# Optimization experiments

Hardware: AMD Instinct MI355X
Metric: run time of the kernel (lower is better)

## Reference

```python
import jax, jax.numpy as jnp
import numpy as np

N_HEAD = 16
D_HEAD = 64
D_MODEL = 1024
QLEN = 1024
BSZ = 4
RLEN = 1024
CONV = 7
SCALE = 1.0 / D_HEAD ** 0.5
NEG = -1e30
EPS = 1e-5


def setup_inputs() -> dict:
    key = jax.random.key(0)
    ks = jax.random.split(key, 14)
    s = 0.02
    inp = {
        "w": jax.random.normal(ks[0], (QLEN, BSZ, D_MODEL), jnp.float32),
        "r": jax.random.normal(ks[1], (RLEN, D_MODEL), jnp.float32),
        "r_w_bias": jax.random.normal(ks[2], (N_HEAD, D_HEAD), jnp.float32) * s,
        "r_r_bias": jax.random.normal(ks[3], (N_HEAD, D_HEAD), jnp.float32) * s,
        "W_qkv": jax.random.normal(ks[4], (3 * N_HEAD * D_HEAD, D_MODEL), jnp.float32) * s,
        "W_r": jax.random.normal(ks[5], (N_HEAD * D_HEAD, D_MODEL), jnp.float32) * s,
        "W_o": jax.random.normal(ks[6], (D_MODEL, N_HEAD * D_HEAD), jnp.float32) * s,
        "conv_wq": jax.random.normal(ks[7], (D_HEAD, D_HEAD, CONV), jnp.float32) * s,
        "conv_bq": jax.random.normal(ks[8], (D_HEAD,), jnp.float32) * s,
        "conv_wk": jax.random.normal(ks[9], (D_HEAD, D_HEAD, CONV), jnp.float32) * s,
        "conv_bk": jax.random.normal(ks[10], (D_HEAD,), jnp.float32) * s,
        "conv_wv": jax.random.normal(ks[11], (D_HEAD, D_HEAD, CONV), jnp.float32) * s,
        "conv_bv": jax.random.normal(ks[12], (D_HEAD,), jnp.float32) * s,
        "ln_gamma": jnp.ones((D_MODEL,), jnp.float32),
        "ln_beta": jnp.zeros((D_MODEL,), jnp.float32),
        # causal mask, True = masked out (original dim==3 branch: [qlen, klen, 1])
        "attn_mask": jnp.triu(jnp.ones((QLEN, QLEN), bool), k=1)[:, :, None],
    }
    return inp


def _conv1d(x, wgt, b):
    # x: [N, C, L], wgt: [O, I, K] (torch Conv1d layout), same padding
    y = jax.lax.conv_general_dilated(x, wgt, (1,), [(CONV // 2, CONV // 2)],
                                     dimension_numbers=("NCH", "OIH", "NCH"))
    return y + b[None, :, None]


def _rel_shift(x):
    # x: [q, k, b, n] -> Transformer-XL relative shift
    q, k, b, n = x.shape
    xp = jnp.concatenate([jnp.zeros((q, 1, b, n), x.dtype), x], axis=1)
    return xp.reshape(k + 1, q, b, n)[1:].reshape(q, k, b, n)


def reference(w, r, r_w_bias, r_r_bias, W_qkv, W_r, W_o,
              conv_wq, conv_bq, conv_wk, conv_bk, conv_wv, conv_bv,
              ln_gamma, ln_beta, attn_mask):
    qlen, bsz, _ = w.shape
    klen = qlen  # mems=None

    heads = jnp.einsum('qbm,hm->qbh', w, W_qkv)  # [q, b, 3*n*d]
    hq, hk, hv = jnp.split(heads, 3, axis=-1)

    def to_conv(x, L):
        # [L, b, n*d] -> [n*b, d, L]
        return x.reshape(L, bsz, N_HEAD, D_HEAD).transpose(2, 1, 3, 0).reshape(N_HEAD * bsz, D_HEAD, L)

    def from_conv(x, L):
        # [n*b, d, L] -> [L, b, n, d]
        return x.reshape(N_HEAD, bsz, D_HEAD, L).transpose(3, 1, 0, 2)

    q_h = from_conv(_conv1d(to_conv(hq, qlen), conv_wq, conv_bq), qlen)
    k_h = from_conv(_conv1d(to_conv(hk, klen), conv_wk, conv_bk), klen)
    v_h = from_conv(_conv1d(to_conv(hv, klen), conv_wv, conv_bv), klen)

    r_head_k = (r @ W_r.T).reshape(-1, N_HEAD, D_HEAD)  # [rlen, n, d]

    AC = jnp.einsum('ibnd,jbnd->ijbn', q_h + r_w_bias, k_h)
    BD = _rel_shift(jnp.einsum('ibnd,jnd->ijbn', q_h + r_r_bias, r_head_k))
    score = (AC + BD) * SCALE
    score = jnp.where(attn_mask[:, :, :, None], NEG, score)

    prob = jax.nn.softmax(score, axis=1)
    vec = jnp.einsum('ijbn,jbnd->ibnd', prob, v_h).reshape(qlen, bsz, N_HEAD * D_HEAD)
    attn_out = vec @ W_o.T

    x = w + attn_out
    mu = jnp.mean(x, axis=-1, keepdims=True)
    var = jnp.mean(jnp.square(x - mu), axis=-1, keepdims=True)
    return (x - mu) / jnp.sqrt(var + EPS) * ln_gamma + ln_beta
```

## Files before the change

kernel.cpp:

```cpp
#include <hip/hip_runtime.h>
#include <math.h>

#define L 1024
#define SCALEF 0.125f
#define NEGF -1e30f

typedef unsigned short u16;
typedef __bf16 bf16x8 __attribute__((ext_vector_type(8)));
typedef float f32x4 __attribute__((ext_vector_type(4)));
typedef unsigned short u16x8 __attribute__((ext_vector_type(8)));
typedef unsigned short u16x4 __attribute__((ext_vector_type(4)));

#define MFMA(a, b, c) __builtin_amdgcn_mfma_f32_16x16x32_bf16(a, b, c, 0, 0, 0)

__device__ inline u16 f2b(float f) {
  union { float f; unsigned u; } v; v.f = f;
  unsigned r = v.u + 0x7fffu + ((v.u >> 16) & 1u);
  return (u16)(r >> 16);
}

__device__ __forceinline__ void ld16(u16* lds, const u16* g) {
  __builtin_amdgcn_global_load_lds((const __attribute__((address_space(1))) unsigned int*)g,
                                   (__attribute__((address_space(3))) unsigned int*)lds, 16, 0, 0);
}

__global__ __launch_bounds__(256) void prep(const float* __restrict__ w, const float* __restrict__ Wqkv,
                                            const float* __restrict__ r, const float* __restrict__ Wr,
                                            const float* __restrict__ Wo,
                                            const float* __restrict__ cwq, const float* __restrict__ cwk,
                                            const float* __restrict__ cwv,
                                            u16* w_bf, u16* wqkv_bf, u16* r_bf, u16* wr_bf, u16* wo_bf,
                                            u16* wTq, u16* wTk, u16* wTv) {
  int i = blockIdx.x * 256 + threadIdx.x;
  if (i < 2621440) {
    const float* s; u16* d; int off;
    if (i < 1048576)      { s = w;    d = w_bf;    off = i; }
    else if (i < 1835008) { s = Wqkv; d = wqkv_bf; off = i - 1048576; }
    else if (i < 2097152) { s = r;    d = r_bf;    off = i - 1835008; }
    else if (i < 2359296) { s = Wr;   d = wr_bf;   off = i - 2097152; }
    else                  { s = Wo;   d = wo_bf;   off = i - 2359296; }
    float4 v = ((const float4*)s)[off];
    u16x4 o = {f2b(v.x), f2b(v.y), f2b(v.z), f2b(v.w)};
    ((u16x4*)d)[off] = o;
  } else {
    int j = i - 2621440;
    if (j < 86016) {
      int z = j / 28672, rem = j % 28672;
      const float* src = z == 0 ? cwq : z == 1 ? cwk : cwv;
      u16* dst = z == 0 ? wTq : z == 1 ? wTk : wTv;
      int tt = rem >> 12, rem2 = rem & 4095;
      int dout = rem2 >> 6, din = rem2 & 63;
      dst[rem] = f2b(src[(dout * 64 + din) * 7 + tt]);
    }
  }
}

template <int OB>
__device__ __forceinline__ void gemm_tile(u16* sA, u16* sB, const u16* A, const u16* B,
                                          void* Cp, int N, int K, int m0, int n0) {
  int t = threadIdx.x;
  int w = t >> 6, lane = t & 63;
  int q4 = lane >> 4, li = lane & 15;
  int mw = (w & 1) << 6, nw = (w >> 1) << 6;
  f32x4 acc[4][4];
#pragma unroll
  for (int i = 0; i < 4; ++i)
#pragma unroll
    for (int j = 0; j < 4; ++j) acc[i][j] = (f32x4){0.f, 0.f, 0.f, 0.f};
  int r0 = t >> 2, c0 = (t & 3) << 3;
  const u16* Ap0 = A + (size_t)(m0 + r0) * K + c0;
  const u16* Ap1 = A + (size_t)(m0 + 64 + r0) * K + c0;
  const u16* Bp0 = B + (size_t)(n0 + r0) * K + c0;
  const u16* Bp1 = B + (size_t)(n0 + 64 + r0) * K + c0;
  int wo512 = w * 512;
  ld16(sA + wo512, Ap0);
  ld16(sA + wo512 + 2048, Ap1);
  ld16(sB + wo512, Bp0);
  ld16(sB + wo512 + 2048, Bp1);
  int cur = 0;
  for (int kb = 0; kb < K; kb += 32) {
    __syncthreads();
    int nxt = cur ^ 1;
    if (kb + 32 < K) {
      u16* nA = sA + nxt * 4096;
      u16* nB = sB + nxt * 4096;
      ld16(nA + wo512, Ap0 + kb + 32);
      ld16(nA + wo512 + 2048, Ap1 + kb + 32);
      ld16(nB + wo512, Bp0 + kb + 32);
      ld16(nB + wo512 + 2048, Bp1 + kb + 32);
    }
    const u16* cA = sA + cur * 4096;
    const u16* cB = sB + cur * 4096;
    bf16x8 fa[4], fb[4];
#pragma unroll
    for (int i = 0; i < 4; ++i) fa[i] = *(const bf16x8*)&cA[(mw + i * 16 + li) * 32 + q4 * 8];
#pragma unroll
    for (int i = 0; i < 4; ++i) fb[i] = *(const bf16x8*)&cB[(nw + i * 16 + li) * 32 + q4 * 8];
#pragma unroll
    for (int mt = 0; mt < 4; ++mt)
#pragma unroll
      for (int nt = 0; nt < 4; ++nt) acc[mt][nt] = MFMA(fa[mt], fb[nt], acc[mt][nt]);
    cur = nxt;
  }
#pragma unroll
  for (int mt = 0; mt < 4; ++mt)
#pragma unroll
    for (int r = 0; r < 4; ++r) {
      size_t row = m0 + mw + mt * 16 + q4 * 4 + r;
      if (OB) {
        u16* C = (u16*)Cp;
#pragma unroll
        for (int nt = 0; nt < 4; ++nt) C[row * N + n0 + nw + nt * 16 + li] = f2b(acc[mt][nt][r]);
      } else {
        float* C = (float*)Cp;
#pragma unroll
        for (int nt = 0; nt < 4; ++nt) C[row * N + n0 + nw + nt * 16 + li] = acc[mt][nt][r];
      }
    }
}

__global__ __launch_bounds__(256) void gemm_stage1(const u16* __restrict__ w_bf, const u16* __restrict__ wqkv_bf,
                                                   u16* __restrict__ heads,
                                                   const u16* __restrict__ r_bf, const u16* __restrict__ wr_bf,
                                                   u16* __restrict__ rhk) {
  __shared__ u16 sA[2 * 128 * 32];
  __shared__ u16 sB[2 * 128 * 32];
  int id = blockIdx.x;
  if (id < 768) {
    gemm_tile<1>(sA, sB, w_bf, wqkv_bf, heads, 3072, 1024, (id / 24) << 7, (id % 24) << 7);
  } else {
    int j = id - 768;
    gemm_tile<1>(sA, sB, r_bf, wr_bf, rhk, 1024, 1024, (j >> 3) << 7, (j & 7) << 7);
  }
}

__global__ __launch_bounds__(256) void gemm_wo(const u16* __restrict__ A, const u16* __restrict__ B,
                                               float* __restrict__ C) {
  __shared__ u16 sA[2 * 64 * 32];
  __shared__ u16 sB[2 * 128 * 32];
  int t = threadIdx.x;
  int w = t >> 6, lane = t & 63;
  int q4 = lane >> 4, li = lane & 15;
  int m0 = blockIdx.y << 6, n0 = blockIdx.x << 7;
  int nw = w << 5;
  const int N = 1024, K = 1024;
  f32x4 acc[4][2];
#pragma unroll
  for (int i = 0; i < 4; ++i)
#pragma unroll
    for (int j = 0; j < 2; ++j) acc[i][j] = (f32x4){0.f, 0.f, 0.f, 0.f};
  int r0 = t >> 2, c0 = (t & 3) << 3;
  const u16* Ap = A + (size_t)(m0 + r0) * K + c0;
  const u16* Bp0 = B + (size_t)(n0 + r0) * K + c0;
  const u16* Bp1 = B + (size_t)(n0 + 64 + r0) * K + c0;
  int wo512 = w * 512;
  ld16(sA + wo512, Ap);
  ld16(sB + wo512, Bp0);
  ld16(sB + wo512 + 2048, Bp1);
  int cur = 0;
  for (int kb = 0; kb < K; kb += 32) {
    __syncthreads();
    int nxt = cur ^ 1;
    if (kb + 32 < K) {
      u16* nA = sA + nxt * 2048;
      u16* nB = sB + nxt * 4096;
      ld16(nA + wo512, Ap + kb + 32);
      ld16(nB + wo512, Bp0 + kb + 32);
      ld16(nB + wo512 + 2048, Bp1 + kb + 32);
    }
    const u16* cA = sA + cur * 2048;
    const u16* cB = sB + cur * 4096;
    bf16x8 fa[4], fb[2];
#pragma unroll
    for (int i = 0; i < 4; ++i) fa[i] = *(const bf16x8*)&cA[(i * 16 + li) * 32 + q4 * 8];
#pragma unroll
    for (int j = 0; j < 2; ++j) fb[j] = *(const bf16x8*)&cB[(nw + j * 16 + li) * 32 + q4 * 8];
#pragma unroll
    for (int mt = 0; mt < 4; ++mt)
#pragma unroll
      for (int nt = 0; nt < 2; ++nt) acc[mt][nt] = MFMA(fa[mt], fb[nt], acc[mt][nt]);
    cur = nxt;
  }
#pragma unroll
  for (int mt = 0; mt < 4; ++mt)
#pragma unroll
    for (int r = 0; r < 4; ++r) {
      size_t row = m0 + mt * 16 + q4 * 4 + r;
#pragma unroll
      for (int nt = 0; nt < 2; ++nt) C[row * N + n0 + nw + nt * 16 + li] = acc[mt][nt][r];
    }
}

__global__ __launch_bounds__(256) void conv3(const u16* __restrict__ x,
                                             const u16* __restrict__ wTq, const u16* __restrict__ wTk,
                                             const u16* __restrict__ wTv,
                                             const float* __restrict__ cbq, const float* __restrict__ cbk,
                                             const float* __restrict__ cbv,
                                             u16* __restrict__ qh, u16* __restrict__ kh, u16* __restrict__ vtg) {
  __shared__ u16 sX[70 * 72];
  int z = blockIdx.z;
  const u16* wT = z == 0 ? wTq : z == 1 ? wTk : wTv;
  const float* bias = z == 0 ? cbq : z == 1 ? cbk : cbv;
  int t = threadIdx.x;
  int w = t >> 6, lane = t & 63;
  int q4 = lane >> 4, li = lane & 15;
  int l0 = blockIdx.x << 6, bn = blockIdx.y;
  int b = bn >> 4, n = bn & 15;
  const u16* xb = x + b * 3072 + z * 1024 + n * 64;
  for (int e = t; e < 560; e += 256) {
    int ro = e >> 3, c = e & 7;
    int l = l0 - 3 + ro;
    u16x8 v = {0, 0, 0, 0, 0, 0, 0, 0};
    if (l >= 0 && l < L) v = *(const u16x8*)(xb + (size_t)l * 12288 + c * 8);
    *(u16x8*)&sX[ro * 72 + c * 8] = v;
  }
  bf16x8 Bw[7][2];
#pragma unroll
  for (int tt = 0; tt < 7; ++tt)
#pragma unroll
    for (int kc = 0; kc < 2; ++kc)
      Bw[tt][kc] = *(const bf16x8*)(wT + (tt * 64 + w * 16 + li) * 64 + kc * 32 + q4 * 8);
  f32x4 acc[4];
#pragma unroll
  for (int i = 0; i < 4; ++i) acc[i] = (f32x4){0.f, 0.f, 0.f, 0.f};
  __syncthreads();
#pragma unroll
  for (int tt = 0; tt < 7; ++tt)
#pragma unroll
    for (int kc = 0; kc < 2; ++kc)
#pragma unroll
      for (int mt = 0; mt < 4; ++mt) {
        bf16x8 a = *(const bf16x8*)&sX[(mt * 16 + li + tt) * 72 + kc * 32 + q4 * 8];
        acc[mt] = MFMA(a, Bw[tt][kc], acc[mt]);
      }
  float bv = bias[w * 16 + li];
  if (z < 2) {
    u16* out = z == 0 ? qh : kh;
#pragma unroll
    for (int mt = 0; mt < 4; ++mt)
#pragma unroll
      for (int r = 0; r < 4; ++r) {
        int l = l0 + mt * 16 + q4 * 4 + r;
        out[(((size_t)l * 4 + b) * 16 + n) * 64 + w * 16 + li] = f2b(acc[mt][r] + bv);
      }
  } else {
    __syncthreads();
#pragma unroll
    for (int mt = 0; mt < 4; ++mt)
#pragma unroll
      for (int r = 0; r < 4; ++r)
        sX[(w * 16 + li) * 72 + mt * 16 + q4 * 4 + r] = f2b(acc[mt][r] + bv);
    __syncthreads();
    int d = t >> 2, ch = t & 3;
    u16x8 v0 = *(u16x8*)&sX[d * 72 + ch * 16];
    u16x8 v1 = *(u16x8*)&sX[d * 72 + ch * 16 + 8];
    u16* dst = vtg + ((size_t)bn * 64 + d) * 1024 + l0 + ch * 16;
    *(u16x8*)dst = v0;
    *(u16x8*)(dst + 8) = v1;
  }
}

__global__ __launch_bounds__(256) void rel_attn(const u16* __restrict__ qh, const u16* __restrict__ kh,
                                                const u16* __restrict__ vt, const u16* __restrict__ rhk,
                                                const float* __restrict__ rwb_, const float* __restrict__ rrb_,
                                                u16* __restrict__ vec) {
  __shared__ u16 sK[64][72];
  __shared__ u16 sVt[64][72];
  __shared__ u16 sR[128][72];
  __shared__ u16 sP[4][16][72];
  int t = threadIdx.x;
  int w = t >> 6, lane = t & 63;
  int q4 = lane >> 4, li = lane & 15;
  int p = blockIdx.x, bn = blockIdx.y;
  int b = bn >> 4, n = bn & 15;
  int base_w = 48 - w * 16;
  const u16* vtb = vt + (size_t)bn * 64 * 1024;
  int er0 = t >> 3, ec = (t & 7) * 8;
  bf16x8 vone;
#pragma unroll
  for (int j = 0; j < 8; ++j) vone[j] = (__bf16)1.0f;
  float rwbv[2][8], rrbv[2][8];
#pragma unroll
  for (int kc = 0; kc < 2; ++kc)
#pragma unroll
    for (int j = 0; j < 8; ++j) {
      int d = kc * 32 + q4 * 8 + j;
      rwbv[kc][j] = rwb_[n * 64 + d];
      rrbv[kc][j] = rrb_[n * 64 + d];
    }
  for (int half = 0; half < 2; ++half) {
    int qt = (half == 0) ? p : 15 - p;
    int i0 = qt << 6;
    bf16x8 Aw[2], Ar[2];
    {
      const u16* qrow = qh + (((size_t)(i0 + w * 16 + li) * 4 + b) * 16 + n) * 64;
#pragma unroll
      for (int kc = 0; kc < 2; ++kc) {
        bf16x8 qv = *(const bf16x8*)(qrow + kc * 32 + q4 * 8);
        bf16x8 aw, ar;
#pragma unroll
        for (int j = 0; j < 8; ++j) {
          float qf = (float)qv[j];
          aw[j] = (__bf16)(qf + rwbv[kc][j]);
          ar[j] = (__bf16)(qf + rrbv[kc][j]);
        }
        Aw[kc] = aw;
        Ar[kc] = ar;
      }
    }
    f32x4 accO[4];
#pragma unroll
    for (int i = 0; i < 4; ++i) accO[i] = (f32x4){0.f, 0.f, 0.f, 0.f};
    f32x4 accL = (f32x4){0.f, 0.f, 0.f, 0.f};
    int ntile = qt + 1;
    u16x8 pK[2], pV[2], pR[4];
    {
      int j0 = 0, gB = 960 - i0;
#pragma unroll
      for (int i = 0; i < 2; ++i) {
        int row = er0 + i * 32;
        pK[i] = *(const u16x8*)(kh + (((size_t)(j0 + row) * 4 + b) * 16 + n) * 64 + ec);
        pV[i] = *(const u16x8*)(vtb + (size_t)row * 1024 + j0 + ec);
      }
#pragma unroll
      for (int i = 0; i < 4; ++i) {
        int m = er0 + i * 32;
        int g = gB + m;
        if (g > L - 1) g = L - 1;
        pR[i] = *(const u16x8*)(rhk + (size_t)g * 1024 + n * 64 + ec);
      }
    }
    for (int jt = 0; jt < ntile; ++jt) {
      __syncthreads();
#pragma unroll
      for (int i = 0; i < 2; ++i) {
        *(u16x8*)&sK[er0 + i * 32][ec] = pK[i];
        *(u16x8*)&sVt[er0 + i * 32][ec] = pV[i];
      }
#pragma unroll
      for (int i = 0; i < 4; ++i) *(u16x8*)&sR[er0 + i * 32][ec] = pR[i];
      __syncthreads();
      if (jt + 1 < ntile) {
        int j0 = (jt + 1) << 6, gB = 960 - i0 + j0;
#pragma unroll
        for (int i = 0; i < 2; ++i) {
          int row = er0 + i * 32;
          pK[i] = *(const u16x8*)(kh + (((size_t)(j0 + row) * 4 + b) * 16 + n) * 64 + ec);
          pV[i] = *(const u16x8*)(vtb + (size_t)row * 1024 + j0 + ec);
        }
#pragma unroll
        for (int i = 0; i < 4; ++i) {
          int m = er0 + i * 32;
          int g = gB + m;
          if (g > L - 1) g = L - 1;
          pR[i] = *(const u16x8*)(rhk + (size_t)g * 1024 + n * 64 + ec);
        }
      }
      int j0 = jt << 6;
      f32x4 accS[4], accG[5];
#pragma unroll
      for (int i = 0; i < 4; ++i) accS[i] = (f32x4){0.f, 0.f, 0.f, 0.f};
#pragma unroll
      for (int i = 0; i < 5; ++i) accG[i] = (f32x4){0.f, 0.f, 0.f, 0.f};
      __builtin_amdgcn_s_setprio(1);
#pragma unroll
      for (int kc = 0; kc < 2; ++kc) {
#pragma unroll
        for (int nt = 0; nt < 4; ++nt) {
          bf16x8 fk = *(const bf16x8*)&sK[nt * 16 + li][kc * 32 + q4 * 8];
          accS[nt] = MFMA(Aw[kc], fk, accS[nt]);
        }
#pragma unroll
        for (int nt = 0; nt < 5; ++nt) {
          bf16x8 fr = *(const bf16x8*)&sR[base_w + nt * 16 + li][kc * 32 + q4 * 8];
          accG[nt] = MFMA(Ar[kc], fr, accG[nt]);
        }
      }
      __builtin_amdgcn_s_setprio(0);
      float Sv[4][4];
#pragma unroll
      for (int nt = 0; nt < 4; ++nt)
#pragma unroll
        for (int r = 0; r < 4; ++r) {
          int il = q4 * 4 + r;
          int srcc = li + 15 - il;
          int lsrc = (lane & 48) | (srcc & 15);
          float pm = (li >= 15 - il) ? accG[nt][r] : accG[nt + 1][r];
          float g = __shfl(pm, lsrc);
          Sv[nt][r] = (accS[nt][r] + g) * SCALEF;
        }
      if (jt == qt) {
#pragma unroll
        for (int nt = 0; nt < 4; ++nt)
#pragma unroll
          for (int r = 0; r < 4; ++r)
            if (j0 + nt * 16 + li > i0 + w * 16 + q4 * 4 + r) Sv[nt][r] = NEGF;
      }
#pragma unroll
      for (int nt = 0; nt < 4; ++nt)
#pragma unroll
        for (int r = 0; r < 4; ++r) {
          float pv = __expf(Sv[nt][r]);
          sP[w][q4 * 4 + r][(nt * 16 + li) ^ (q4 << 3)] = f2b(pv);
        }
      __builtin_amdgcn_s_setprio(1);
#pragma unroll
      for (int kc = 0; kc < 2; ++kc) {
        bf16x8 ap = *(const bf16x8*)&sP[w][li][kc * 32 + ((q4 ^ ((li >> 2) & 3)) << 3)];
        accL = MFMA(ap, vone, accL);
#pragma unroll
        for (int nt = 0; nt < 4; ++nt) {
          bf16x8 fv = *(const bf16x8*)&sVt[nt * 16 + li][kc * 32 + q4 * 8];
          accO[nt] = MFMA(ap, fv, accO[nt]);
        }
      }
      __builtin_amdgcn_s_setprio(0);
    }
#pragma unroll
    for (int r = 0; r < 4; ++r) {
      int il = q4 * 4 + r;
      int ig = i0 + w * 16 + il;
      float inv = 1.0f / accL[r];
      u16* orow = vec + (((size_t)ig * 4 + b) * 16 + n) * 64;
#pragma unroll
      for (int nt = 0; nt < 4; ++nt) orow[nt * 16 + li] = f2b(accO[nt][r] * inv);
    }
  }
}

__global__ __launch_bounds__(256) void resid_ln(const float* __restrict__ w,
                                                const float* __restrict__ attn,
                                                const float* __restrict__ gamma,
                                                const float* __restrict__ beta,
                                                float* __restrict__ out) {
  __shared__ float ssum[4], ssq[4];
  int row = blockIdx.x, t = threadIdx.x;
  float4 xw = *(const float4*)&w[(size_t)row * 1024 + t * 4];
  float4 xa = *(const float4*)&attn[(size_t)row * 1024 + t * 4];
  float4 x = make_float4(xw.x + xa.x, xw.y + xa.y, xw.z + xa.z, xw.w + xa.w);
  float s = x.x + x.y + x.z + x.w;
  float sq = x.x * x.x + x.y * x.y + x.z * x.z + x.w * x.w;
#pragma unroll
  for (int off = 32; off > 0; off >>= 1) {
    s += __shfl_down(s, off);
    sq += __shfl_down(sq, off);
  }
  int wid = t >> 6;
  if ((t & 63) == 0) { ssum[wid] = s; ssq[wid] = sq; }
  __syncthreads();
  s = ssum[0] + ssum[1] + ssum[2] + ssum[3];
  sq = ssq[0] + ssq[1] + ssq[2] + ssq[3];
  float mean = s * (1.0f / 1024.0f);
  float var = sq * (1.0f / 1024.0f) - mean * mean;
  float rstd = rsqrtf(var + 1e-5f);
  float4 g = *(const float4*)&gamma[t * 4];
  float4 bb = *(const float4*)&beta[t * 4];
  float4 o;
  o.x = (x.x - mean) * rstd * g.x + bb.x;
  o.y = (x.y - mean) * rstd * g.y + bb.y;
  o.z = (x.z - mean) * rstd * g.z + bb.z;
  o.w = (x.w - mean) * rstd * g.w + bb.w;
  *(float4*)&out[(size_t)row * 1024 + t * 4] = o;
}

extern "C" void kernel_launch(void* const* d_in, const int* in_sizes, int n_in,
                              void* d_out, int out_size, void* d_ws, size_t ws_size,
                              hipStream_t stream) {
  const float* w     = (const float*)d_in[0];
  const float* r     = (const float*)d_in[1];
  const float* rwb   = (const float*)d_in[2];
  const float* rrb   = (const float*)d_in[3];
  const float* W_qkv = (const float*)d_in[4];
  const float* W_r   = (const float*)d_in[5];
  const float* W_o   = (const float*)d_in[6];
  const float* cwq   = (const float*)d_in[7];
  const float* cbq   = (const float*)d_in[8];
  const float* cwk   = (const float*)d_in[9];
  const float* cbk   = (const float*)d_in[10];
  const float* cwv   = (const float*)d_in[11];
  const float* cbv   = (const float*)d_in[12];
  const float* gamma = (const float*)d_in[13];
  const float* beta  = (const float*)d_in[14];
  float* outp = (float*)d_out;

  char* wsb = (char*)d_ws;
  u16*   heads   = (u16*)(wsb);
  u16*   vec     = (u16*)(wsb);
  float* attnf   = (float*)(wsb + 8388608);
  u16*   qh      = (u16*)(wsb + 25165824);
  u16*   kh      = (u16*)(wsb + 33554432);
  u16*   rhk     = (u16*)(wsb + 50331648);
  u16*   w_bf    = (u16*)(wsb + 52428800);
  u16*   wqkv_bf = (u16*)(wsb + 60817408);
  u16*   r_bf    = (u16*)(wsb + 67108864);
  u16*   wr_bf   = (u16*)(wsb + 69206016);
  u16*   wo_bf   = (u16*)(wsb + 71303168);
  u16*   wTq     = (u16*)(wsb + 73400320);
  u16*   wTk     = (u16*)(wsb + 73457664);
  u16*   wTv     = (u16*)(wsb + 73515008);
  u16*   vt      = (u16*)(wsb + 73572352);

  dim3 blk(256);
  prep<<<10576, blk, 0, stream>>>(w, W_qkv, r, W_r, W_o, cwq, cwk, cwv,
                                  w_bf, wqkv_bf, r_bf, wr_bf, wo_bf, wTq, wTk, wTv);
  gemm_stage1<<<832, blk, 0, stream>>>(w_bf, wqkv_bf, heads, r_bf, wr_bf, rhk);
  conv3<<<dim3(16, 64, 3), blk, 0, stream>>>(heads, wTq, wTk, wTv, cbq, cbk, cbv, qh, kh, vt);
  rel_attn<<<dim3(8, 64), blk, 0, stream>>>(qh, kh, vt, rhk, rwb, rrb, vec);
  gemm_wo<<<dim3(8, 64), blk, 0, stream>>>(vec, wo_bf, attnf);
  resid_ln<<<4096, blk, 0, stream>>>(w, attnf, gamma, beta, outp);
}
```

Measured before the change: 261.9 us.

## Rewrite stage-1 GEMM with 256x256 tiles, 4-stage LDS pipeline and swizzle

Replaces the 128x128 double-buffered GEMM tile for the QKV and R projections with a 256x256 tile computed by 512 threads (8 waves). It uses a 4-slot LDS ring with explicit vmcnt waits, an XOR swizzle on LDS columns to avoid bank conflicts, and s_setprio around the MFMA bursts. The aim is more data reuse per loaded byte and better overlap of global loads with MFMA. In exchange the grid drops to 208 blocks, fewer than two per CU, and the kernel uses 128KB of LDS per block with one block per CU, so load balance and occupancy may suffer.

```diff
diff --git a/kernel.cpp b/kernel.cpp
--- a/kernel.cpp
+++ b/kernel.cpp
@@ -56,81 +56,97 @@
 }
 
 template <int OB>
-__device__ __forceinline__ void gemm_tile(u16* sA, u16* sB, const u16* A, const u16* B,
-                                          void* Cp, int N, int K, int m0, int n0) {
+__device__ __forceinline__ void gemm256_tile(u16* lds, const u16* __restrict__ A,
+                                             const u16* __restrict__ B, void* Cp,
+                                             int N, int m0, int n0) {
   int t = threadIdx.x;
-  int w = t >> 6, lane = t & 63;
+  int wv = t >> 6, lane = t & 63;
   int q4 = lane >> 4, li = lane & 15;
-  int mw = (w & 1) << 6, nw = (w >> 1) << 6;
-  f32x4 acc[4][4];
-#pragma unroll
-  for (int i = 0; i < 4; ++i)
-#pragma unroll
-    for (int j = 0; j < 4; ++j) acc[i][j] = (f32x4){0.f, 0.f, 0.f, 0.f};
-  int r0 = t >> 2, c0 = (t & 3) << 3;
-  const u16* Ap0 = A + (size_t)(m0 + r0) * K + c0;
-  const u16* Ap1 = A + (size_t)(m0 + 64 + r0) * K + c0;
-  const u16* Bp0 = B + (size_t)(n0 + r0) * K + c0;
-  const u16* Bp1 = B + (size_t)(n0 + 64 + r0) * K + c0;
-  int wo512 = w * 512;
-  ld16(sA + wo512, Ap0);
-  ld16(sA + wo512 + 2048, Ap1);
-  ld16(sB + wo512, Bp0);
-  ld16(sB + wo512 + 2048, Bp1);
-  int cur = 0;
-  for (int kb = 0; kb < K; kb += 32) {
-    __syncthreads();
-    int nxt = cur ^ 1;
-    if (kb + 32 < K) {
-      u16* nA = sA + nxt * 4096;
-      u16* nB = sB + nxt * 4096;
-      ld16(nA + wo512, Ap0 + kb + 32);
-      ld16(nA + wo512 + 2048, Ap1 + kb + 32);
-      ld16(nB + wo512, Bp0 + kb + 32);
-      ld16(nB + wo512 + 2048, Bp1 + kb + 32);
-    }
-    const u16* cA = sA + cur * 4096;
-    const u16* cB = sB + cur * 4096;
+  int wm = wv >> 2, wn = wv & 3;
+  int pc = (q4 ^ ((li >> 1) & 3)) << 3;
+  int cs = (((t & 3) ^ ((t >> 3) & 3)) << 3);
+  const u16* Ab = A + (size_t)(m0 + (t >> 2)) * 1024 + cs;
+  const u16* Bb = B + (size_t)(n0 + (t >> 2)) * 1024 + cs;
+  int wo = wv * 512;
+  f32x4 acc[8][4];
+#pragma unroll
+  for (int m = 0; m < 8; ++m)
+#pragma unroll
+    for (int n = 0; n < 4; ++n) acc[m][n] = (f32x4){0.f, 0.f, 0.f, 0.f};
+#define STAGE_A(kt) { int sl = ((kt) & 3) * 16384, kb = (kt) * 32; \
+    ld16(lds + sl + wo, Ab + kb); ld16(lds + sl + 4096 + wo, Ab + 131072 + kb); }
+#define STAGE_B(kt) { int sl = ((kt) & 3) * 16384 + 8192, kb = (kt) * 32; \
+    ld16(lds + sl + wo, Bb + kb); ld16(lds + sl + 4096 + wo, Bb + 131072 + kb); }
+  STAGE_A(0); STAGE_B(0); STAGE_A(1); STAGE_B(1);
+  asm volatile("s_waitcnt vmcnt(4)" ::: "memory");
+  __builtin_amdgcn_s_barrier();
+  for (int kt = 0; kt < 32; ++kt) {
+    const u16* sA = lds + (kt & 3) * 16384;
+    const u16* sB = sA + 8192;
     bf16x8 fa[4], fb[4];
 #pragma unroll
-    for (int i = 0; i < 4; ++i) fa[i] = *(const bf16x8*)&cA[(mw + i * 16 + li) * 32 + q4 * 8];
-#pragma unroll
-    for (int i = 0; i < 4; ++i) fb[i] = *(const bf16x8*)&cB[(nw + i * 16 + li) * 32 + q4 * 8];
-#pragma unroll
-    for (int mt = 0; mt < 4; ++mt)
-#pragma unroll
-      for (int nt = 0; nt < 4; ++nt) acc[mt][nt] = MFMA(fa[mt], fb[nt], acc[mt][nt]);
-    cur = nxt;
-  }
-#pragma unroll
-  for (int mt = 0; mt < 4; ++mt)
+    for (int m = 0; m < 4; ++m) fa[m] = *(const bf16x8*)&sA[(wm * 128 + m * 16 + li) * 32 + pc];
+#pragma unroll
+    for (int n = 0; n < 4; ++n) fb[n] = *(const bf16x8*)&sB[(wn * 64 + n * 16 + li) * 32 + pc];
+    if (kt < 30) STAGE_A(kt + 2);
+    __builtin_amdgcn_s_barrier();
+    __builtin_amdgcn_s_setprio(1);
+#pragma unroll
+    for (int m = 0; m < 4; ++m)
+#pragma unroll
+      for (int n = 0; n < 4; ++n) acc[m][n] = MFMA(fa[m], fb[n], acc[m][n]);
+    __builtin_amdgcn_s_setprio(0);
+    __builtin_amdgcn_s_barrier();
+    bf16x8 fa2[4];
+#pragma unroll
+    for (int m = 0; m < 4; ++m) fa2[m] = *(const bf16x8*)&sA[(wm * 128 + 64 + m * 16 + li) * 32 + pc];
+    if (kt < 30) {
+      STAGE_B(kt + 2);
+      asm volatile("s_waitcnt vmcnt(4)" ::: "memory");
+    } else {
+      asm volatile("s_waitcnt vmcnt(0)" ::: "memory");
+    }
+    __builtin_amdgcn_s_barrier();
+    __builtin_amdgcn_s_setprio(1);
+#pragma unroll
+    for (int m = 0; m < 4; ++m)
+#pragma unroll
+      for (int n = 0; n < 4; ++n) acc[4 + m][n] = MFMA(fa2[m], fb[n], acc[4 + m][n]);
+    __builtin_amdgcn_s_setprio(0);
+    __builtin_amdgcn_s_barrier();
+  }
+#undef STAGE_A
+#undef STAGE_B
+#pragma unroll
+  for (int m = 0; m < 8; ++m)
 #pragma unroll
     for (int r = 0; r < 4; ++r) {
-      size_t row = m0 + mw + mt * 16 + q4 * 4 + r;
+      size_t row = m0 + wm * 128 + m * 16 + q4 * 4 + r;
       if (OB) {
         u16* C = (u16*)Cp;
 #pragma unroll
-        for (int nt = 0; nt < 4; ++nt) C[row * N + n0 + nw + nt * 16 + li] = f2b(acc[mt][nt][r]);
+        for (int n = 0; n < 4; ++n) C[row * N + n0 + wn * 64 + n * 16 + li] = f2b(acc[m][n][r]);
       } else {
         float* C = (float*)Cp;
 #pragma unroll
-        for (int nt = 0; nt < 4; ++nt) C[row * N + n0 + nw + nt * 16 + li] = acc[mt][nt][r];
-      }
-    }
-}
-
-__global__ __launch_bounds__(256) void gemm_stage1(const u16* __restrict__ w_bf, const u16* __restrict__ wqkv_bf,
-                                                   u16* __restrict__ heads,
-                                                   const u16* __restrict__ r_bf, const u16* __restrict__ wr_bf,
-                                                   u16* __restrict__ rhk) {
-  __shared__ u16 sA[2 * 128 * 32];
-  __shared__ u16 sB[2 * 128 * 32];
+        for (int n = 0; n < 4; ++n) C[row * N + n0 + wn * 64 + n * 16 + li] = acc[m][n][r];
+      }
+    }
+}
+
+__global__ __launch_bounds__(512, 1) void gemm_stage1(const u16* __restrict__ w_bf,
+                                                      const u16* __restrict__ wqkv_bf,
+                                                      u16* __restrict__ heads,
+                                                      const u16* __restrict__ r_bf,
+                                                      const u16* __restrict__ wr_bf,
+                                                      u16* __restrict__ rhk) {
+  __shared__ u16 lds[65536];
   int id = blockIdx.x;
-  if (id < 768) {
-    gemm_tile<1>(sA, sB, w_bf, wqkv_bf, heads, 3072, 1024, (id / 24) << 7, (id % 24) << 7);
+  if (id < 192) {
+    gemm256_tile<1>(lds, w_bf, wqkv_bf, heads, 3072, (id / 12) << 8, (id % 12) << 8);
   } else {
-    int j = id - 768;
-    gemm_tile<1>(sA, sB, r_bf, wr_bf, rhk, 1024, 1024, (j >> 3) << 7, (j & 7) << 7);
+    int j = id - 192;
+    gemm256_tile<1>(lds, r_bf, wr_bf, rhk, 1024, (j >> 2) << 8, (j & 3) << 8);
   }
 }
 
@@ -503,7 +519,7 @@
   dim3 blk(256);
   prep<<<10576, blk, 0, stream>>>(w, W_qkv, r, W_r, W_o, cwq, cwk, cwv,
                                   w_bf, wqkv_bf, r_bf, wr_bf, wo_bf, wTq, wTk, wTv);
-  gemm_stage1<<<832, blk, 0, stream>>>(w_bf, wqkv_bf, heads, r_bf, wr_bf, rhk);
+  gemm_stage1<<<208, dim3(512), 0, stream>>>(w_bf, wqkv_bf, heads, r_bf, wr_bf, rhk);
   conv3<<<dim3(16, 64, 3), blk, 0, stream>>>(heads, wTq, wTk, wTv, cbq, cbk, cbv, qh, kh, vt);
   rel_attn<<<dim3(8, 64), blk, 0, stream>>>(qh, kh, vt, rhk, rwb, rrb, vec);
   gemm_wo<<<dim3(8, 64), blk, 0, stream>>>(vec, wo_bf, attnf);
```

Measured after the change: 249.9 us. -4.6%, faster.
